# Performance work log

Measured on AMD Instinct MI355X. Metric: run time of the kernel, lower is better.

## Reference

```python
import jax, jax.numpy as jnp
import numpy as np

WIN = 3      # win_h = win_w = 3 (required for the reshape in the original code)
DIL = 1      # dilation; unfold padding == dilation in the original module
CUT = 0.0    # self.cut is hard-set to 0 in __init__


def _l2norm(x):
    # torch F.normalize(dim=1, p=2): x / max(||x||_2, eps)
    n = jnp.sqrt(jnp.sum(x * x, axis=1, keepdims=True))
    return x / jnp.maximum(n, 1e-12)


def setup_inputs() -> dict:
    key = jax.random.key(0)
    k1, k2 = jax.random.split(key)
    image = jax.random.normal(k1, (4, 64, 256, 256), dtype=jnp.float32)
    event = jax.random.normal(k2, (4, 64, 256, 256), dtype=jnp.float32)
    return {"image": image, "event": event}


def reference(image, event):
    B, C, H, W = image.shape
    img = _l2norm(image)
    ev = _l2norm(event)

    pad = DIL  # unfold padding == dilation
    imgp = jnp.pad(img, ((0, 0), (0, 0), (pad, pad), (pad, pad)))

    # NOTE: the original code unfolds `image` for BOTH branches (event_neighbor
    # is also built from image) -- we reproduce that faithfully.
    outs = []
    for i in range(WIN):
        for j in range(WIN):
            if i == WIN // 2 and j == WIN // 2:
                continue  # center element (index num = win_h*win_w//2) dropped
            nb = imgp[:, :, i * DIL:i * DIL + H, j * DIL:j * DIL + W]  # [B,C,H,W]
            # sum over channels of (nb * img) * (nb * ev)
            outs.append(jnp.sum((nb * img) * (nb * ev), axis=1))  # [B,H,W]
    aff = jnp.stack(outs, axis=1)  # [B, win_h*win_w - 1, H, W]
    # affinity[affinity < cut] = cut with cut == 0
    return jnp.maximum(aff, CUT)
```

## Files before the change

kernel.cpp:

```cpp
#include <hip/hip_runtime.h>

#define NB 4
#define NC 64
#define NH 256
#define NW 256
#define HW (NH * NW)
#define WAVES 8
#define CPW 8

__device__ __forceinline__ float4 f4zero() { return make_float4(0.f, 0.f, 0.f, 0.f); }

__global__ __launch_bounds__(512) void k_fused(
    const float* __restrict__ img, const float* __restrict__ ev,
    float* __restrict__ out)
{
    __shared__ float red[2][48][64];

    const int lane = threadIdx.x & 63;
    const int wv   = threadIdx.x >> 6;

    const int bid = blockIdx.x;
    const int swz = (bid & 7) * 128 + (bid >> 3);
    const int b = swz >> 8;
    const int h = swz & 255;
    const int w = lane << 2;

    const bool hm = (h > 0);
    const bool hp = (h < NH - 1);

    const size_t base = (size_t)b * NC * HW + (size_t)(wv * CPW) * HW
                      + (size_t)h * NW + w;
    const float* ibase = img + base;
    const float* ebase = ev + base;

    float acc[8][4];
    float si[3][4];
    float se[4];
#pragma unroll
    for (int k = 0; k < 8; ++k)
#pragma unroll
        for (int x = 0; x < 4; ++x) acc[k][x] = 0.f;
#pragma unroll
    for (int r = 0; r < 3; ++r)
#pragma unroll
        for (int x = 0; x < 4; ++x) si[r][x] = 0.f;
#pragma unroll
    for (int x = 0; x < 4; ++x) se[x] = 0.f;

#pragma unroll 2
    for (int c = 0; c < CPW; ++c) {
        const float* p = ibase + (size_t)c * HW;
        float4 zm = hm ? *(const float4*)(p - NW) : f4zero();
        float4 zz = *(const float4*)(p);
        float4 zp = hp ? *(const float4*)(p + NW) : f4zero();
        float4 ee = *(const float4*)(ebase + (size_t)c * HW);

        float lm = __shfl_up(zm.w, 1);
        float lz = __shfl_up(zz.w, 1);
        float lp = __shfl_up(zp.w, 1);
        float rm = __shfl_down(zm.x, 1);
        float rz = __shfl_down(zz.x, 1);
        float rp = __shfl_down(zp.x, 1);
        if (lane == 0)  { lm = 0.f; lz = 0.f; lp = 0.f; }
        if (lane == 63) { rm = 0.f; rz = 0.f; rp = 0.f; }

        float m6[6] = { lm, zm.x, zm.y, zm.z, zm.w, rm };
        float z6[6] = { lz, zz.x, zz.y, zz.z, zz.w, rz };
        float p6[6] = { lp, zp.x, zp.y, zp.z, zp.w, rp };
        float sqm[6], sqz[6], sqp[6];
#pragma unroll
        for (int i = 0; i < 6; ++i) {
            sqm[i] = m6[i] * m6[i];
            sqz[i] = z6[i] * z6[i];
            sqp[i] = p6[i] * p6[i];
        }
#pragma unroll
        for (int x = 0; x < 4; ++x) {
            si[0][x] += sqm[x + 1];
            si[1][x] += sqz[x + 1];
            si[2][x] += sqp[x + 1];
        }
        se[0] = fmaf(ee.x, ee.x, se[0]);
        se[1] = fmaf(ee.y, ee.y, se[1]);
        se[2] = fmaf(ee.z, ee.z, se[2]);
        se[3] = fmaf(ee.w, ee.w, se[3]);

        float pe[4] = { z6[1] * ee.x, z6[2] * ee.y, z6[3] * ee.z, z6[4] * ee.w };
#pragma unroll
        for (int x = 0; x < 4; ++x) {
            acc[0][x] = fmaf(sqm[x],     pe[x], acc[0][x]);
            acc[1][x] = fmaf(sqm[x + 1], pe[x], acc[1][x]);
            acc[2][x] = fmaf(sqm[x + 2], pe[x], acc[2][x]);
            acc[3][x] = fmaf(sqz[x],     pe[x], acc[3][x]);
            acc[4][x] = fmaf(sqz[x + 2], pe[x], acc[4][x]);
            acc[5][x] = fmaf(sqp[x],     pe[x], acc[5][x]);
            acc[6][x] = fmaf(sqp[x + 1], pe[x], acc[6][x]);
            acc[7][x] = fmaf(sqp[x + 2], pe[x], acc[7][x]);
        }
    }

#define STORE_VALS(slot)                                                     \
    {                                                                        \
        for (int k = 0; k < 8; ++k)                                          \
            for (int x = 0; x < 4; ++x) red[slot][k * 4 + x][lane] = acc[k][x]; \
        for (int r = 0; r < 3; ++r)                                          \
            for (int x = 0; x < 4; ++x) red[slot][32 + r * 4 + x][lane] = si[r][x]; \
        for (int x = 0; x < 4; ++x) red[slot][44 + x][lane] = se[x];         \
    }
#define ADD_VALS(slot)                                                       \
    {                                                                        \
        for (int k = 0; k < 8; ++k)                                          \
            for (int x = 0; x < 4; ++x) acc[k][x] += red[slot][k * 4 + x][lane]; \
        for (int r = 0; r < 3; ++r)                                          \
            for (int x = 0; x < 4; ++x) si[r][x] += red[slot][32 + r * 4 + x][lane]; \
        for (int x = 0; x < 4; ++x) se[x] += red[slot][44 + x][lane];        \
    }

    if (wv == 4) STORE_VALS(0);
    if (wv == 5) STORE_VALS(1);
    __syncthreads();
    if (wv == 0) ADD_VALS(0);
    if (wv == 1) ADD_VALS(1);
    __syncthreads();
    if (wv == 6) STORE_VALS(0);
    if (wv == 7) STORE_VALS(1);
    __syncthreads();
    if (wv == 2) ADD_VALS(0);
    if (wv == 3) ADD_VALS(1);
    __syncthreads();
    if (wv == 2) STORE_VALS(0);
    if (wv == 3) STORE_VALS(1);
    __syncthreads();
    if (wv == 0) ADD_VALS(0);
    if (wv == 1) ADD_VALS(1);
    __syncthreads();
    if (wv == 1) STORE_VALS(0);
    __syncthreads();
    if (wv != 0) return;
    ADD_VALS(0);
#undef STORE_VALS
#undef ADD_VALS

    float rnm[4], rnz[4], rnp[4], rne[4];
#pragma unroll
    for (int x = 0; x < 4; ++x) {
        rnm[x] = 1.f / fmaxf(sqrtf(si[0][x]), 1e-12f);
        rnz[x] = 1.f / fmaxf(sqrtf(si[1][x]), 1e-12f);
        rnp[x] = 1.f / fmaxf(sqrtf(si[2][x]), 1e-12f);
        rne[x] = 1.f / fmaxf(sqrtf(se[x]), 1e-12f);
    }

    float lnm = __shfl_up(rnm[3], 1);
    float lnz = __shfl_up(rnz[3], 1);
    float lnp = __shfl_up(rnp[3], 1);
    float rnm_ = __shfl_down(rnm[0], 1);
    float rnz_ = __shfl_down(rnz[0], 1);
    float rnp_ = __shfl_down(rnp[0], 1);
    if (lane == 0)  { lnm = 0.f; lnz = 0.f; lnp = 0.f; }
    if (lane == 63) { rnm_ = 0.f; rnz_ = 0.f; rnp_ = 0.f; }

    float nm6[6] = { lnm, rnm[0], rnm[1], rnm[2], rnm[3], rnm_ };
    float nz6[6] = { lnz, rnz[0], rnz[1], rnz[2], rnz[3], rnz_ };
    float np6[6] = { lnp, rnp[0], rnp[1], rnp[2], rnp[3], rnp_ };

    float ctr[4];
#pragma unroll
    for (int x = 0; x < 4; ++x) ctr[x] = nz6[x + 1] * rne[x];

    float* outp = out + (((size_t)b * 8) * NH + h) * NW + w;
#pragma unroll
    for (int k = 0; k < 8; ++k) {
        float nbv[4];
#pragma unroll
        for (int x = 0; x < 4; ++x) {
            float v;
            switch (k) {
                case 0: v = nm6[x];     break;
                case 1: v = nm6[x + 1]; break;
                case 2: v = nm6[x + 2]; break;
                case 3: v = nz6[x];     break;
                case 4: v = nz6[x + 2]; break;
                case 5: v = np6[x];     break;
                case 6: v = np6[x + 1]; break;
                default: v = np6[x + 2]; break;
            }
            nbv[x] = v;
        }
        float4 o;
        o.x = fmaxf(acc[k][0] * (nbv[0] * nbv[0]) * ctr[0], 0.f);
        o.y = fmaxf(acc[k][1] * (nbv[1] * nbv[1]) * ctr[1], 0.f);
        o.z = fmaxf(acc[k][2] * (nbv[2] * nbv[2]) * ctr[2], 0.f);
        o.w = fmaxf(acc[k][3] * (nbv[3] * nbv[3]) * ctr[3], 0.f);
        *(float4*)(outp + (size_t)k * NH * NW) = o;
    }
}

extern "C" void kernel_launch(void* const* d_in, const int* in_sizes, int n_in,
                              void* d_out, int out_size, void* d_ws, size_t ws_size,
                              hipStream_t stream) {
    (void)in_sizes; (void)n_in; (void)out_size; (void)d_ws; (void)ws_size;
    const float* img = (const float*)d_in[0];
    const float* ev  = (const float*)d_in[1];
    float* out = (float*)d_out;

    k_fused<<<NB * NH, 512, 0, stream>>>(img, ev, out);
}
```

Before: 34.14 us.

## Process four rows per block with four channel-split waves each

Each 1024-thread block now handles four output rows, with four waves per row splitting the 64 channels into groups of 16 instead of eight waves of 8 channels on one row. This shortens the shared-memory tree reduction to two levels and cuts the grid to a quarter as many blocks. Boundary-row loads are also made unconditional by clamping the offset and multiplying by a 0/1 mask, which removes branches around the loads. The larger block raises shared-memory use to 96 KB and register pressure under launch_bounds(1024), which may limit occupancy.

```diff
diff --git a/kernel.cpp b/kernel.cpp
--- a/kernel.cpp
+++ b/kernel.cpp
@@ -5,37 +5,38 @@
 #define NH 256
 #define NW 256
 #define HW (NH * NW)
-#define WAVES 8
-#define CPW 8
+#define RPB 4
+#define CPW 16
 
-__device__ __forceinline__ float4 f4zero() { return make_float4(0.f, 0.f, 0.f, 0.f); }
-
-__global__ __launch_bounds__(512) void k_fused(
+__global__ __launch_bounds__(1024) void k_fused(
     const float* __restrict__ img, const float* __restrict__ ev,
     float* __restrict__ out)
 {
-    __shared__ float red[2][48][64];
+    __shared__ float red[RPB][2][48][64];
 
     const int lane = threadIdx.x & 63;
     const int wv   = threadIdx.x >> 6;
+    const int row  = wv >> 2;
+    const int q    = wv & 3;
 
     const int bid = blockIdx.x;
-    const int swz = (bid & 7) * 128 + (bid >> 3);
-    const int b = swz >> 8;
-    const int h = swz & 255;
-    const int w = lane << 2;
+    const int swz = (bid & 7) * 32 + (bid >> 3);
+    const int b   = swz >> 6;
+    const int h0  = (swz & 63) << 2;
+    const int h   = h0 + row;
+    const int w   = lane << 2;
 
-    const bool hm = (h > 0);
-    const bool hp = (h < NH - 1);
+    const float hmf = (h > 0) ? 1.f : 0.f;
+    const float hpf = (h < NH - 1) ? 1.f : 0.f;
+    const int offm = (h > 0) ? -NW : 0;
+    const int offp = (h < NH - 1) ? NW : 0;
 
-    const size_t base = (size_t)b * NC * HW + (size_t)(wv * CPW) * HW
+    const size_t base = (size_t)b * NC * HW + (size_t)(q * CPW) * HW
                       + (size_t)h * NW + w;
     const float* ibase = img + base;
     const float* ebase = ev + base;
 
-    float acc[8][4];
-    float si[3][4];
-    float se[4];
+    float acc[8][4], si[3][4], se[4];
 #pragma unroll
     for (int k = 0; k < 8; ++k)
 #pragma unroll
@@ -50,23 +51,25 @@
 #pragma unroll 2
     for (int c = 0; c < CPW; ++c) {
         const float* p = ibase + (size_t)c * HW;
-        float4 zm = hm ? *(const float4*)(p - NW) : f4zero();
-        float4 zz = *(const float4*)(p);
-        float4 zp = hp ? *(const float4*)(p + NW) : f4zero();
-        float4 ee = *(const float4*)(ebase + (size_t)c * HW);
+        float4 M = *(const float4*)(p + offm);
+        float4 Z = *(const float4*)(p);
+        float4 P = *(const float4*)(p + offp);
+        float4 E = *(const float4*)(ebase + (size_t)c * HW);
+        M.x *= hmf; M.y *= hmf; M.z *= hmf; M.w *= hmf;
+        P.x *= hpf; P.y *= hpf; P.z *= hpf; P.w *= hpf;
 
-        float lm = __shfl_up(zm.w, 1);
-        float lz = __shfl_up(zz.w, 1);
-        float lp = __shfl_up(zp.w, 1);
-        float rm = __shfl_down(zm.x, 1);
-        float rz = __shfl_down(zz.x, 1);
-        float rp = __shfl_down(zp.x, 1);
+        float lm = __shfl_up(M.w, 1);
+        float lz = __shfl_up(Z.w, 1);
+        float lp = __shfl_up(P.w, 1);
+        float rm = __shfl_down(M.x, 1);
+        float rz = __shfl_down(Z.x, 1);
+        float rp = __shfl_down(P.x, 1);
         if (lane == 0)  { lm = 0.f; lz = 0.f; lp = 0.f; }
         if (lane == 63) { rm = 0.f; rz = 0.f; rp = 0.f; }
 
-        float m6[6] = { lm, zm.x, zm.y, zm.z, zm.w, rm };
-        float z6[6] = { lz, zz.x, zz.y, zz.z, zz.w, rz };
-        float p6[6] = { lp, zp.x, zp.y, zp.z, zp.w, rp };
+        float m6[6] = { lm, M.x, M.y, M.z, M.w, rm };
+        float z6[6] = { lz, Z.x, Z.y, Z.z, Z.w, rz };
+        float p6[6] = { lp, P.x, P.y, P.z, P.w, rp };
         float sqm[6], sqz[6], sqp[6];
 #pragma unroll
         for (int i = 0; i < 6; ++i) {
@@ -80,12 +83,12 @@
             si[1][x] += sqz[x + 1];
             si[2][x] += sqp[x + 1];
         }
-        se[0] = fmaf(ee.x, ee.x, se[0]);
-        se[1] = fmaf(ee.y, ee.y, se[1]);
-        se[2] = fmaf(ee.z, ee.z, se[2]);
-        se[3] = fmaf(ee.w, ee.w, se[3]);
+        se[0] = fmaf(E.x, E.x, se[0]);
+        se[1] = fmaf(E.y, E.y, se[1]);
+        se[2] = fmaf(E.z, E.z, se[2]);
+        se[3] = fmaf(E.w, E.w, se[3]);
 
-        float pe[4] = { z6[1] * ee.x, z6[2] * ee.y, z6[3] * ee.z, z6[4] * ee.w };
+        float pe[4] = { z6[1] * E.x, z6[2] * E.y, z6[3] * E.z, z6[4] * E.w };
 #pragma unroll
         for (int x = 0; x < 4; ++x) {
             acc[0][x] = fmaf(sqm[x],     pe[x], acc[0][x]);
@@ -102,41 +105,29 @@
 #define STORE_VALS(slot)                                                     \
     {                                                                        \
         for (int k = 0; k < 8; ++k)                                          \
-            for (int x = 0; x < 4; ++x) red[slot][k * 4 + x][lane] = acc[k][x]; \
+            for (int x = 0; x < 4; ++x) red[row][slot][k * 4 + x][lane] = acc[k][x]; \
         for (int r = 0; r < 3; ++r)                                          \
-            for (int x = 0; x < 4; ++x) red[slot][32 + r * 4 + x][lane] = si[r][x]; \
-        for (int x = 0; x < 4; ++x) red[slot][44 + x][lane] = se[x];         \
+            for (int x = 0; x < 4; ++x) red[row][slot][32 + r * 4 + x][lane] = si[r][x]; \
+        for (int x = 0; x < 4; ++x) red[row][slot][44 + x][lane] = se[x];    \
     }
 #define ADD_VALS(slot)                                                       \
     {                                                                        \
         for (int k = 0; k < 8; ++k)                                          \
-            for (int x = 0; x < 4; ++x) acc[k][x] += red[slot][k * 4 + x][lane]; \
+            for (int x = 0; x < 4; ++x) acc[k][x] += red[row][slot][k * 4 + x][lane]; \
         for (int r = 0; r < 3; ++r)                                          \
-            for (int x = 0; x < 4; ++x) si[r][x] += red[slot][32 + r * 4 + x][lane]; \
-        for (int x = 0; x < 4; ++x) se[x] += red[slot][44 + x][lane];        \
+            for (int x = 0; x < 4; ++x) si[r][x] += red[row][slot][32 + r * 4 + x][lane]; \
+        for (int x = 0; x < 4; ++x) se[x] += red[row][slot][44 + x][lane];   \
     }
 
-    if (wv == 4) STORE_VALS(0);
-    if (wv == 5) STORE_VALS(1);
+    if (q == 2) STORE_VALS(0);
+    if (q == 3) STORE_VALS(1);
     __syncthreads();
-    if (wv == 0) ADD_VALS(0);
-    if (wv == 1) ADD_VALS(1);
+    if (q == 0) ADD_VALS(0);
+    if (q == 1) ADD_VALS(1);
     __syncthreads();
-    if (wv == 6) STORE_VALS(0);
-    if (wv == 7) STORE_VALS(1);
+    if (q == 1) STORE_VALS(0);
     __syncthreads();
-    if (wv == 2) ADD_VALS(0);
-    if (wv == 3) ADD_VALS(1);
-    __syncthreads();
-    if (wv == 2) STORE_VALS(0);
-    if (wv == 3) STORE_VALS(1);
-    __syncthreads();
-    if (wv == 0) ADD_VALS(0);
-    if (wv == 1) ADD_VALS(1);
-    __syncthreads();
-    if (wv == 1) STORE_VALS(0);
-    __syncthreads();
-    if (wv != 0) return;
+    if (q != 0) return;
     ADD_VALS(0);
 #undef STORE_VALS
 #undef ADD_VALS
@@ -203,5 +194,5 @@
     const float* ev  = (const float*)d_in[1];
     float* out = (float*)d_out;
 
-    k_fused<<<NB * NH, 512, 0, stream>>>(img, ev, out);
+    k_fused<<<NB * (NH / RPB), 1024, 0, stream>>>(img, ev, out);
 }
```

Measured after the change: 31.17 us. 1.1x faster.
